# Kernel optimization log

Measured on AMD Instinct MI355X. Metric: run time of the kernel, lower is better.

## Reference

```python
import jax, jax.numpy as jnp
import numpy as np

B, T = 256, 256
D_TEXT, D_AUDIO, D_VISION = 300, 74, 35
D = D_TEXT + D_AUDIO + D_VISION  # 409
H = 1024
CELL = 512
OUT = 1


def setup_inputs() -> dict:
    key = jax.random.key(0)
    ks = jax.random.split(key, 8)
    s_ih = 1.0 / np.sqrt(H)
    return {
        "x_text": jax.random.normal(ks[0], (B, T, D_TEXT), jnp.float32),
        "x_audio": jax.random.normal(ks[1], (B, T, D_AUDIO), jnp.float32),
        "x_vision": jax.random.normal(ks[2], (B, T, D_VISION), jnp.float32),
        "W_ih": jax.random.normal(ks[3], (4 * H, D), jnp.float32) * s_ih,
        "W_hh": jax.random.normal(ks[4], (4 * H, H), jnp.float32) * s_ih,
        "b_ih": jnp.zeros((4 * H,), jnp.float32),
        "b_hh": jnp.zeros((4 * H,), jnp.float32),
        "W1": jax.random.normal(ks[5], (CELL, H), jnp.float32) / np.sqrt(H),
        "b1": jnp.zeros((CELL,), jnp.float32),
        "W2": jax.random.normal(ks[6], (OUT, CELL), jnp.float32) / np.sqrt(CELL),
        "b2": jnp.zeros((OUT,), jnp.float32),
    }


def _lstm_mlp(x_text, x_audio, x_vision, W_ih, W_hh, b_ih, b_hh, W1, b1, W2, b2):
    # concat modalities along feature dim: [B, T, D]
    x = jnp.concatenate([x_text, x_audio, x_vision], axis=2)
    b = x.shape[0]
    h0 = jnp.zeros((b, H), x.dtype)
    c0 = jnp.zeros((b, H), x.dtype)
    # precompute input-to-gate projection for all timesteps: [T, B, 4H]
    xg = jnp.einsum('btd,gd->tbg', x, W_ih) + (b_ih + b_hh)

    def step(carry, xg_t):
        h, c = carry
        gates = xg_t + h @ W_hh.T  # [B, 4H]
        i, f, g, o = jnp.split(gates, 4, axis=-1)  # PyTorch LSTMCell gate order
        i = jax.nn.sigmoid(i)
        f = jax.nn.sigmoid(f)
        g = jnp.tanh(g)
        o = jax.nn.sigmoid(o)
        c = f * c + i * g
        h = o * jnp.tanh(c)
        return (h, c), None

    (h_last, _), _ = jax.lax.scan(step, (h0, c0), xg)
    # SimpleNet: Linear -> ReLU -> Dropout(eval: identity) -> Linear
    hidden = jax.nn.relu(h_last @ W1.T + b1)
    return hidden @ W2.T + b2  # [B, OUT]


def reference(x_text, x_audio, x_vision, W_ih, W_hh, b_ih, b_hh, W1, b1, W2, b2):
    return _lstm_mlp(x_text, x_audio, x_vision, W_ih, W_hh, b_ih, b_hh, W1, b1, W2, b2)
```

## Files before the change

### kernel.cpp

```cpp
#include <hip/hip_runtime.h>
#include <cstdint>
#include <cstddef>


typedef __attribute__((ext_vector_type(8))) short short8;
typedef __attribute__((ext_vector_type(4))) float f32x4;

#define MFMA_BF16(A,B,C) __builtin_amdgcn_mfma_f32_16x16x32_bf16((A),(B),(C),0,0,0)

#define OFF_FLAGS 0u
#define OFF_HBUF0 4096u
#define OFF_CBUF  528384u
#define ZERO_SPAN 1576960u
#define OFF_HBUF1 1576960u
#define OFF_HFIN  2101248u
#define OFF_HID   3149824u
#define OFF_BIAS  3674112u
#define OFF_WHH   3690496u
#define OFF_WIH   12079104u
#define OFF_XB    15486976u
#define OFF_XG    70012928u
#define WS_NEED   137121792ull

static __device__ __forceinline__ uint16_t f2bf(float f) {
  uint32_t u = __builtin_bit_cast(uint32_t, f);
  uint32_t r = u + 0x7FFFu + ((u >> 16) & 1u);
  return (uint16_t)(r >> 16);
}
static __device__ __forceinline__ float bf2f_lo(uint32_t u) {
  return __builtin_bit_cast(float, u << 16);
}
static __device__ __forceinline__ float bf2f_hi(uint32_t u) {
  return __builtin_bit_cast(float, u & 0xFFFF0000u);
}
static __device__ __forceinline__ float sigm(float x) {
  return 1.0f / (1.0f + __expf(-x));
}
static __device__ __forceinline__ float tanh_f(float x) {
  float e = __expf(2.0f * x);
  return 1.0f - 2.0f / (e + 1.0f);
}
static __device__ __forceinline__ void gld_lds16_coh(const void* gsrc, void* ldst) {
  __builtin_amdgcn_global_load_lds(
      (const __attribute__((address_space(1))) uint32_t*)gsrc,
      (__attribute__((address_space(3))) uint32_t*)ldst, 16, 0, 0x11);
}

__global__ __launch_bounds__(256) void pack_xb_kernel(
    const float* __restrict__ xt, const float* __restrict__ xa,
    const float* __restrict__ xv, uint16_t* __restrict__ xb)
{
  int id = blockIdx.x * 256 + threadIdx.x;
  int lane = id & 63;
  int rem  = id >> 6;
  int ks = rem % 13;
  int mt = rem / 13;
  int m = mt * 16 + (lane & 15);
  int t = m >> 8;
  int b = m & 255;
  int k0 = ks * 32 + (lane >> 4) * 8;
  size_t base = (size_t)b * 256 + t;
  uint16_t vals[8];
#pragma unroll
  for (int e = 0; e < 8; ++e) {
    int k = k0 + e;
    float v;
    if (k < 300)      v = xt[base * 300 + k];
    else if (k < 374) v = xa[base * 74  + (k - 300)];
    else if (k < 409) v = xv[base * 35  + (k - 374)];
    else              v = 0.0f;
    vals[e] = f2bf(v);
  }
  uint32_t* d32 = (uint32_t*)(xb + (size_t)id * 8);
#pragma unroll
  for (int i = 0; i < 4; ++i)
    d32[i] = (uint32_t)vals[2*i] | ((uint32_t)vals[2*i+1] << 16);
}

__global__ __launch_bounds__(256) void pack_whh_kernel(
    const float* __restrict__ whh, uint16_t* __restrict__ wp)
{
  int id = blockIdx.x * 256 + threadIdx.x;
  int lane = id & 63;
  int ks = (id >> 6) & 31;
  int q  = (id >> 11) & 3;
  int s  = id >> 13;
  int row = q * 1024 + s * 16 + (lane & 15);
  int k0 = ks * 32 + (lane >> 4) * 8;
  const float* src = whh + (size_t)row * 1024 + k0;
  uint16_t vals[8];
#pragma unroll
  for (int e = 0; e < 8; ++e) vals[e] = f2bf(src[e]);
  uint32_t* d32 = (uint32_t*)(wp + (size_t)id * 8);
#pragma unroll
  for (int i = 0; i < 4; ++i)
    d32[i] = (uint32_t)vals[2*i] | ((uint32_t)vals[2*i+1] << 16);
}

__global__ __launch_bounds__(256) void pack_wih_kernel(
    const float* __restrict__ wih, uint16_t* __restrict__ wp)
{
  int id = blockIdx.x * 256 + threadIdx.x;
  int lane = id & 63;
  int rem = id >> 6;
  int ks = rem % 13;
  int nt = rem / 13;
  int n = nt * 16 + (lane & 15);
  int k0 = ks * 32 + (lane >> 4) * 8;
  uint16_t vals[8];
#pragma unroll
  for (int e = 0; e < 8; ++e) {
    int k = k0 + e;
    vals[e] = (k < 409) ? f2bf(wih[(size_t)n * 409 + k]) : (uint16_t)0;
  }
  uint32_t* d32 = (uint32_t*)(wp + (size_t)id * 8);
#pragma unroll
  for (int i = 0; i < 4; ++i)
    d32[i] = (uint32_t)vals[2*i] | ((uint32_t)vals[2*i+1] << 16);
}

__global__ __launch_bounds__(256) void pack_bias_kernel(
    const float* __restrict__ b_ih, const float* __restrict__ b_hh,
    float* __restrict__ bias)
{
  int id = blockIdx.x * 256 + threadIdx.x;
  bias[id] = b_ih[id] + b_hh[id];
}

__global__ __launch_bounds__(256) void xg_gemm_kernel(
    const short8* __restrict__ xb, const short8* __restrict__ wih,
    const float* __restrict__ bias, uint2* __restrict__ xg, int chunk)
{
  int tid = threadIdx.x;
  int lane = tid & 63;
  int w = tid >> 6;
  int wm = w & 1, wn = w >> 1;
  int bm = blockIdx.x, bn = blockIdx.y;
  int mtb = bm * 8 + wm * 4;
  int ntb = bn * 8 + wn * 4;
  int col = lane & 15;

  f32x4 acc[4][4];
#pragma unroll
  for (int b = 0; b < 4; ++b) {
    float bv = bias[(ntb + b) * 16 + col];
    f32x4 v = {bv, bv, bv, bv};
#pragma unroll
    for (int a = 0; a < 4; ++a) acc[a][b] = v;
  }
  size_t mt_glob = (size_t)chunk * 512 + mtb;
  for (int ks = 0; ks < 13; ++ks) {
    short8 Af[4], Bf[4];
#pragma unroll
    for (int a = 0; a < 4; ++a)
      Af[a] = xb[((mt_glob + a) * 13 + ks) * 64 + lane];
#pragma unroll
    for (int b = 0; b < 4; ++b)
      Bf[b] = wih[(((size_t)(ntb + b)) * 13 + ks) * 64 + lane];
#pragma unroll
    for (int a = 0; a < 4; ++a)
#pragma unroll
      for (int b = 0; b < 4; ++b)
        acc[a][b] = MFMA_BF16(Af[a], Bf[b], acc[a][b]);
  }
#pragma unroll
  for (int a = 0; a < 4; ++a) {
    int mt = mtb + a;
    int t_loc = mt >> 4;
    int bt = mt & 15;
#pragma unroll
    for (int b = 0; b < 4; ++b) {
      size_t idx = (((size_t)t_loc * 256 + (ntb + b)) * 16 + bt) * 64 + lane;
      f32x4 v = acc[a][b];
      uint2 o;
      o.x = (uint32_t)f2bf(v[0]) | ((uint32_t)f2bf(v[1]) << 16);
      o.y = (uint32_t)f2bf(v[2]) | ((uint32_t)f2bf(v[3]) << 16);
      xg[idx] = o;
    }
  }
}

__global__ __launch_bounds__(256, 1) void scan_kernel(
    const uint16_t* __restrict__ whh_p, const uint2* __restrict__ xg,
    uint16_t* __restrict__ hbuf0, uint16_t* __restrict__ hbuf1,
    float* __restrict__ c_buf, float* __restrict__ h_final,
    uint32_t* flags, int chunk)
{
  extern __shared__ char smem[];
  float* gl = (float*)(smem + 131072);

  const int tid = threadIdx.x;
  const int bid = blockIdx.x;
  const int g = bid >> 6, s = bid & 63;
  const int lane = tid & 63, w = tid >> 6;

  const short8* wstream = (const short8*)(whh_p + (size_t)s * 65536)
                          + ((size_t)w * 32) * 64 + lane;

  const int row_e = tid >> 2;
  const int j_e = (tid & 3) * 4;
  const int R_e = g * 64 + row_e;
  const int col_e = s * 16 + j_e;
  f32x4 c4 = *(const f32x4*)(c_buf + (size_t)R_e * 1024 + col_e);

  size_t hstore_base;
  {
    int cg0 = col_e;
    int ksh = cg0 >> 5, quad = (cg0 >> 3) & 3, e0 = cg0 & 7;
    int mth = row_e >> 4;
    int laneh = quad * 16 + (row_e & 15);
    hstore_base = (((size_t)(g * 4 + mth) * 32 + ksh) * 64 + laneh) * 8 + e0;
  }

  const short8* Afrag = (const short8*)smem;
  const int myflag = g * 64 + lane;

  uint2 xp[4];
#pragma unroll
  for (int a = 0; a < 4; ++a)
    xp[a] = xg[(((size_t)0 * 256 + (w * 64 + s)) * 16 + (g * 4 + a)) * 64 + lane];

  for (int l = 0; l < 32; ++l) {
    const int ts = chunk * 32 + l;
    const uint16_t* hin = (ts & 1) ? hbuf1 : hbuf0;
    uint16_t* hout = (ts & 1) ? hbuf0 : hbuf1;

    {
      const uint16_t* gbase = hin + (size_t)g * 65536
                              + (size_t)(w * 32) * 512 + (size_t)lane * 8;
      char* lbase = smem + (size_t)(w * 32) * 1024;
#pragma unroll
      for (int p = 0; p < 32; ++p)
        gld_lds16_coh(gbase + (size_t)p * 512, lbase + p * 1024);
    }

    f32x4 acc[4];
#pragma unroll
    for (int a = 0; a < 4; ++a) {
      uint2 p = xp[a];
      f32x4 v = {bf2f_lo(p.x), bf2f_hi(p.x), bf2f_lo(p.y), bf2f_hi(p.y)};
      acc[a] = v;
    }

    __syncthreads();

#pragma unroll
    for (int ks = 0; ks < 32; ++ks) {
      short8 W = wstream[ks * 64];
      short8 A0 = Afrag[(0 * 32 + ks) * 64 + lane];
      short8 A1 = Afrag[(1 * 32 + ks) * 64 + lane];
      short8 A2 = Afrag[(2 * 32 + ks) * 64 + lane];
      short8 A3 = Afrag[(3 * 32 + ks) * 64 + lane];
      acc[0] = MFMA_BF16(A0, W, acc[0]);
      acc[1] = MFMA_BF16(A1, W, acc[1]);
      acc[2] = MFMA_BF16(A2, W, acc[2]);
      acc[3] = MFMA_BF16(A3, W, acc[3]);
    }

    {
      int r0 = (lane >> 4) * 4;
      int cc = lane & 15;
      int colc = w * 16 + cc;
#pragma unroll
      for (int a = 0; a < 4; ++a)
#pragma unroll
        for (int r = 0; r < 4; ++r)
          gl[(a * 16 + r0 + r) * 68 + colc] = acc[a][r];
    }
    __syncthreads();

    float hv[4];
#pragma unroll
    for (int u = 0; u < 4; ++u) {
      int cj = j_e + u;
      float xi = gl[row_e * 68 + cj];
      float xf = gl[row_e * 68 + 16 + cj];
      float xg_ = gl[row_e * 68 + 32 + cj];
      float xo = gl[row_e * 68 + 48 + cj];
      float cn = sigm(xf) * c4[u] + sigm(xi) * tanh_f(xg_);
      c4[u] = cn;
      hv[u] = sigm(xo) * tanh_f(cn);
    }
    {
      uint32_t w0 = (uint32_t)f2bf(hv[0]) | ((uint32_t)f2bf(hv[1]) << 16);
      uint32_t w1 = (uint32_t)f2bf(hv[2]) | ((uint32_t)f2bf(hv[3]) << 16);
      unsigned long long v = ((unsigned long long)w1 << 32) | w0;
      __hip_atomic_store((unsigned long long*)(hout + hstore_base), v,
                         __ATOMIC_RELAXED, __HIP_MEMORY_SCOPE_AGENT);
    }
    if (chunk == 7 && l == 31) {
      f32x4 hh = {hv[0], hv[1], hv[2], hv[3]};
      *(f32x4*)(h_final + (size_t)R_e * 1024 + col_e) = hh;
    }
    if (l != 31) {
      __syncthreads();
      if (tid == 0) {
        __hip_atomic_store(&flags[bid], (uint32_t)(ts + 1),
                           __ATOMIC_RELAXED, __HIP_MEMORY_SCOPE_AGENT);
      }
      {
        int ln = l + 1;
#pragma unroll
        for (int a = 0; a < 4; ++a)
          xp[a] = xg[(((size_t)ln * 256 + (w * 64 + s)) * 16 + (g * 4 + a)) * 64 + lane];
      }
      while (__hip_atomic_load(&flags[myflag], __ATOMIC_RELAXED,
                               __HIP_MEMORY_SCOPE_AGENT) < (uint32_t)(ts + 1)) {
        __builtin_amdgcn_s_sleep(1);
      }
    }
  }
  *(f32x4*)(c_buf + (size_t)R_e * 1024 + col_e) = c4;
}

__global__ __launch_bounds__(256) void mlp1_kernel(
    const float* __restrict__ h_final, const float* __restrict__ W1,
    const float* __restrict__ b1, float* __restrict__ hidden)
{
  __shared__ float hl[8 * 1024];
  __shared__ float part[4 * 64 * 8];
  int tid = threadIdx.x;
  int rb = blockIdx.x;
  int cb = blockIdx.y;
  const f32x4* hsrc = (const f32x4*)(h_final + (size_t)rb * 8 * 1024);
  for (int i = tid; i < 2048; i += 256) ((f32x4*)hl)[i] = hsrc[i];
  __syncthreads();
  int cell_l = tid & 63;
  int kq = tid >> 6;
  int cell = cb * 64 + cell_l;
  float accv[8] = {0,0,0,0,0,0,0,0};
  const f32x4* wrow = (const f32x4*)(W1 + (size_t)cell * 1024) + kq * 64;
  const f32x4* hl4 = (const f32x4*)hl;
  for (int k4 = 0; k4 < 64; ++k4) {
    f32x4 wv = wrow[k4];
    int kidx = kq * 64 + k4;
#pragma unroll
    for (int r = 0; r < 8; ++r) {
      f32x4 hv = hl4[r * 256 + kidx];
      accv[r] += wv[0] * hv[0] + wv[1] * hv[1] + wv[2] * hv[2] + wv[3] * hv[3];
    }
  }
#pragma unroll
  for (int r = 0; r < 8; ++r) part[(kq * 64 + cell_l) * 8 + r] = accv[r];
  __syncthreads();
#pragma unroll
  for (int rr = 0; rr < 2; ++rr) {
    int r = kq * 2 + rr;
    float sum = b1[cell];
    for (int q = 0; q < 4; ++q) sum += part[(q * 64 + cell_l) * 8 + r];
    hidden[(size_t)(rb * 8 + r) * 512 + cell] = fmaxf(sum, 0.0f);
  }
}

__global__ __launch_bounds__(256) void mlp2_kernel(
    const float* __restrict__ hidden, const float* __restrict__ W2,
    const float* __restrict__ b2, float* __restrict__ out)
{
  __shared__ float w2l[512];
  int tid = threadIdx.x;
  for (int i = tid; i < 512; i += 256) w2l[i] = W2[i];
  __syncthreads();
  const f32x4* hrow = (const f32x4*)(hidden + (size_t)tid * 512);
  const f32x4* w4 = (const f32x4*)w2l;
  float acc = b2[0];
  for (int k = 0; k < 128; ++k) {
    f32x4 a = hrow[k], b = w4[k];
    acc += a[0] * b[0] + a[1] * b[1] + a[2] * b[2] + a[3] * b[3];
  }
  out[tid] = acc;
}

extern "C" void kernel_launch(void* const* d_in, const int* in_sizes, int n_in,
                              void* d_out, int out_size, void* d_ws, size_t ws_size,
                              hipStream_t stream)
{
  (void)in_sizes; (void)n_in; (void)out_size;
  if (ws_size < WS_NEED) return;

  const float* xt   = (const float*)d_in[0];
  const float* xa   = (const float*)d_in[1];
  const float* xv   = (const float*)d_in[2];
  const float* W_ih = (const float*)d_in[3];
  const float* W_hh = (const float*)d_in[4];
  const float* b_ih = (const float*)d_in[5];
  const float* b_hh = (const float*)d_in[6];
  const float* W1   = (const float*)d_in[7];
  const float* b1   = (const float*)d_in[8];
  const float* W2   = (const float*)d_in[9];
  const float* b2   = (const float*)d_in[10];
  float* out = (float*)d_out;
  char* ws = (char*)d_ws;

  uint32_t* flags   = (uint32_t*)(ws + OFF_FLAGS);
  uint16_t* hb0     = (uint16_t*)(ws + OFF_HBUF0);
  uint16_t* hb1     = (uint16_t*)(ws + OFF_HBUF1);
  float*    c_buf   = (float*)(ws + OFF_CBUF);
  float*    h_final = (float*)(ws + OFF_HFIN);
  float*    hidden  = (float*)(ws + OFF_HID);
  float*    bias    = (float*)(ws + OFF_BIAS);
  uint16_t* whh_p   = (uint16_t*)(ws + OFF_WHH);
  uint16_t* wih_p   = (uint16_t*)(ws + OFF_WIH);
  uint16_t* xb      = (uint16_t*)(ws + OFF_XB);
  uint2*    xg      = (uint2*)(ws + OFF_XG);

  hipFuncSetAttribute((const void*)scan_kernel,
                      hipFuncAttributeMaxDynamicSharedMemorySize, 148480);

  hipMemsetAsync(ws, 0, ZERO_SPAN, stream);

  pack_xb_kernel  <<<13312, 256, 0, stream>>>(xt, xa, xv, xb);
  pack_whh_kernel <<<2048,  256, 0, stream>>>(W_hh, whh_p);
  pack_wih_kernel <<<832,   256, 0, stream>>>(W_ih, wih_p);
  pack_bias_kernel<<<16,    256, 0, stream>>>(b_ih, b_hh, bias);

  for (int c = 0; c < 8; ++c) {
    xg_gemm_kernel<<<dim3(64, 32), 256, 0, stream>>>(
        (const short8*)xb, (const short8*)wih_p, bias, xg, c);
    scan_kernel<<<256, 256, 148480, stream>>>(
        whh_p, xg, hb0, hb1, c_buf, h_final, flags, c);
  }
  mlp1_kernel<<<dim3(32, 8), 256, 0, stream>>>(h_final, W1, b1, hidden);
  mlp2_kernel<<<1, 256, 0, stream>>>(hidden, W2, b2, out);
}
```

Before: 2.038 ms.

## Fuse input projection GEMM into persistent LSTM scan kernel

Removes the separate xg_gemm kernel and its chunked launch loop. The scan kernel now keeps W_ih fragments in registers and computes each timestep's input projection with MFMAs while it waits on the cross-block flag. Everything runs in one persistent launch over 256 timesteps. This drops the xg workspace round trip, seven kernel relaunches and the c_buf save and restore, at the cost of extra registers and extra MFMA work between recurrent steps.

```diff
diff --git a/kernel.cpp b/kernel.cpp
--- a/kernel.cpp
+++ b/kernel.cpp
@@ -10,28 +10,20 @@
 
 #define OFF_FLAGS 0u
 #define OFF_HBUF0 4096u
-#define OFF_CBUF  528384u
-#define ZERO_SPAN 1576960u
-#define OFF_HBUF1 1576960u
-#define OFF_HFIN  2101248u
-#define OFF_HID   3149824u
-#define OFF_BIAS  3674112u
-#define OFF_WHH   3690496u
-#define OFF_WIH   12079104u
-#define OFF_XB    15486976u
-#define OFF_XG    70012928u
-#define WS_NEED   137121792ull
+#define ZERO_SPAN 528384u
+#define OFF_HBUF1 528384u
+#define OFF_HFIN  1052672u
+#define OFF_HID   2101248u
+#define OFF_BIAS  2625536u
+#define OFF_WHH   2641920u
+#define OFF_WIH   11030528u
+#define OFF_XB    14438400u
+#define WS_NEED   68964352ull
 
 static __device__ __forceinline__ uint16_t f2bf(float f) {
   uint32_t u = __builtin_bit_cast(uint32_t, f);
   uint32_t r = u + 0x7FFFu + ((u >> 16) & 1u);
   return (uint16_t)(r >> 16);
-}
-static __device__ __forceinline__ float bf2f_lo(uint32_t u) {
-  return __builtin_bit_cast(float, u << 16);
-}
-static __device__ __forceinline__ float bf2f_hi(uint32_t u) {
-  return __builtin_bit_cast(float, u & 0xFFFF0000u);
 }
 static __device__ __forceinline__ float sigm(float x) {
   return 1.0f / (1.0f + __expf(-x));
@@ -127,64 +119,11 @@
   bias[id] = b_ih[id] + b_hh[id];
 }
 
-__global__ __launch_bounds__(256) void xg_gemm_kernel(
-    const short8* __restrict__ xb, const short8* __restrict__ wih,
-    const float* __restrict__ bias, uint2* __restrict__ xg, int chunk)
-{
-  int tid = threadIdx.x;
-  int lane = tid & 63;
-  int w = tid >> 6;
-  int wm = w & 1, wn = w >> 1;
-  int bm = blockIdx.x, bn = blockIdx.y;
-  int mtb = bm * 8 + wm * 4;
-  int ntb = bn * 8 + wn * 4;
-  int col = lane & 15;
-
-  f32x4 acc[4][4];
-#pragma unroll
-  for (int b = 0; b < 4; ++b) {
-    float bv = bias[(ntb + b) * 16 + col];
-    f32x4 v = {bv, bv, bv, bv};
-#pragma unroll
-    for (int a = 0; a < 4; ++a) acc[a][b] = v;
-  }
-  size_t mt_glob = (size_t)chunk * 512 + mtb;
-  for (int ks = 0; ks < 13; ++ks) {
-    short8 Af[4], Bf[4];
-#pragma unroll
-    for (int a = 0; a < 4; ++a)
-      Af[a] = xb[((mt_glob + a) * 13 + ks) * 64 + lane];
-#pragma unroll
-    for (int b = 0; b < 4; ++b)
-      Bf[b] = wih[(((size_t)(ntb + b)) * 13 + ks) * 64 + lane];
-#pragma unroll
-    for (int a = 0; a < 4; ++a)
-#pragma unroll
-      for (int b = 0; b < 4; ++b)
-        acc[a][b] = MFMA_BF16(Af[a], Bf[b], acc[a][b]);
-  }
-#pragma unroll
-  for (int a = 0; a < 4; ++a) {
-    int mt = mtb + a;
-    int t_loc = mt >> 4;
-    int bt = mt & 15;
-#pragma unroll
-    for (int b = 0; b < 4; ++b) {
-      size_t idx = (((size_t)t_loc * 256 + (ntb + b)) * 16 + bt) * 64 + lane;
-      f32x4 v = acc[a][b];
-      uint2 o;
-      o.x = (uint32_t)f2bf(v[0]) | ((uint32_t)f2bf(v[1]) << 16);
-      o.y = (uint32_t)f2bf(v[2]) | ((uint32_t)f2bf(v[3]) << 16);
-      xg[idx] = o;
-    }
-  }
-}
-
 __global__ __launch_bounds__(256, 1) void scan_kernel(
-    const uint16_t* __restrict__ whh_p, const uint2* __restrict__ xg,
+    const uint16_t* __restrict__ whh_p, const short8* __restrict__ xb,
+    const short8* __restrict__ wih, const float* __restrict__ bias,
     uint16_t* __restrict__ hbuf0, uint16_t* __restrict__ hbuf1,
-    float* __restrict__ c_buf, float* __restrict__ h_final,
-    uint32_t* flags, int chunk)
+    float* __restrict__ h_final, uint32_t* flags)
 {
   extern __shared__ char smem[];
   float* gl = (float*)(smem + 131072);
@@ -201,7 +140,7 @@
   const int j_e = (tid & 3) * 4;
   const int R_e = g * 64 + row_e;
   const int col_e = s * 16 + j_e;
-  f32x4 c4 = *(const f32x4*)(c_buf + (size_t)R_e * 1024 + col_e);
+  f32x4 c4 = {0.0f, 0.0f, 0.0f, 0.0f};
 
   size_t hstore_base;
   {
@@ -215,13 +154,29 @@
   const short8* Afrag = (const short8*)smem;
   const int myflag = g * 64 + lane;
 
-  uint2 xp[4];
-#pragma unroll
-  for (int a = 0; a < 4; ++a)
-    xp[a] = xg[(((size_t)0 * 256 + (w * 64 + s)) * 16 + (g * 4 + a)) * 64 + lane];
-
-  for (int l = 0; l < 32; ++l) {
-    const int ts = chunk * 32 + l;
+  const int nt = w * 64 + s;
+  short8 Bih[13];
+  {
+    const short8* bsrc = wih + ((size_t)nt * 13) * 64 + lane;
+#pragma unroll
+    for (int ks = 0; ks < 13; ++ks) Bih[ks] = bsrc[ks * 64];
+  }
+  const float bv = bias[nt * 16 + (lane & 15)];
+
+  f32x4 xacc[4];
+  {
+    const short8* abase = xb + (((size_t)g * 4) * 13) * 64 + lane;
+#pragma unroll
+    for (int a = 0; a < 4; ++a) { f32x4 v = {bv, bv, bv, bv}; xacc[a] = v; }
+#pragma unroll
+    for (int ks = 0; ks < 13; ++ks)
+#pragma unroll
+      for (int a = 0; a < 4; ++a)
+        xacc[a] = MFMA_BF16(abase[((size_t)a * 13 + ks) * 64], Bih[ks], xacc[a]);
+  }
+
+#pragma unroll 1
+  for (int ts = 0; ts < 256; ++ts) {
     const uint16_t* hin = (ts & 1) ? hbuf1 : hbuf0;
     uint16_t* hout = (ts & 1) ? hbuf0 : hbuf1;
 
@@ -236,11 +191,7 @@
 
     f32x4 acc[4];
 #pragma unroll
-    for (int a = 0; a < 4; ++a) {
-      uint2 p = xp[a];
-      f32x4 v = {bf2f_lo(p.x), bf2f_hi(p.x), bf2f_lo(p.y), bf2f_hi(p.y)};
-      acc[a] = v;
-    }
+    for (int a = 0; a < 4; ++a) acc[a] = xacc[a];
 
     __syncthreads();
 
@@ -288,21 +239,26 @@
       __hip_atomic_store((unsigned long long*)(hout + hstore_base), v,
                          __ATOMIC_RELAXED, __HIP_MEMORY_SCOPE_AGENT);
     }
-    if (chunk == 7 && l == 31) {
+    if (ts == 255) {
       f32x4 hh = {hv[0], hv[1], hv[2], hv[3]};
       *(f32x4*)(h_final + (size_t)R_e * 1024 + col_e) = hh;
-    }
-    if (l != 31) {
+    } else {
       __syncthreads();
       if (tid == 0) {
         __hip_atomic_store(&flags[bid], (uint32_t)(ts + 1),
                            __ATOMIC_RELAXED, __HIP_MEMORY_SCOPE_AGENT);
       }
       {
-        int ln = l + 1;
-#pragma unroll
-        for (int a = 0; a < 4; ++a)
-          xp[a] = xg[(((size_t)ln * 256 + (w * 64 + s)) * 16 + (g * 4 + a)) * 64 + lane];
+        const short8* abase =
+            xb + (((size_t)(ts + 1) * 16 + g * 4) * 13) * 64 + lane;
+#pragma unroll
+        for (int a = 0; a < 4; ++a) { f32x4 v = {bv, bv, bv, bv}; xacc[a] = v; }
+#pragma unroll
+        for (int ks = 0; ks < 13; ++ks)
+#pragma unroll
+          for (int a = 0; a < 4; ++a)
+            xacc[a] =
+                MFMA_BF16(abase[((size_t)a * 13 + ks) * 64], Bih[ks], xacc[a]);
       }
       while (__hip_atomic_load(&flags[myflag], __ATOMIC_RELAXED,
                                __HIP_MEMORY_SCOPE_AGENT) < (uint32_t)(ts + 1)) {
@@ -310,7 +266,6 @@
       }
     }
   }
-  *(f32x4*)(c_buf + (size_t)R_e * 1024 + col_e) = c4;
 }
 
 __global__ __launch_bounds__(256) void mlp1_kernel(
@@ -394,14 +349,12 @@
   uint32_t* flags   = (uint32_t*)(ws + OFF_FLAGS);
   uint16_t* hb0     = (uint16_t*)(ws + OFF_HBUF0);
   uint16_t* hb1     = (uint16_t*)(ws + OFF_HBUF1);
-  float*    c_buf   = (float*)(ws + OFF_CBUF);
   float*    h_final = (float*)(ws + OFF_HFIN);
   float*    hidden  = (float*)(ws + OFF_HID);
   float*    bias    = (float*)(ws + OFF_BIAS);
   uint16_t* whh_p   = (uint16_t*)(ws + OFF_WHH);
   uint16_t* wih_p   = (uint16_t*)(ws + OFF_WIH);
   uint16_t* xb      = (uint16_t*)(ws + OFF_XB);
-  uint2*    xg      = (uint2*)(ws + OFF_XG);
 
   hipFuncSetAttribute((const void*)scan_kernel,
                       hipFuncAttributeMaxDynamicSharedMemorySize, 148480);
@@ -413,12 +366,10 @@
   pack_wih_kernel <<<832,   256, 0, stream>>>(W_ih, wih_p);
   pack_bias_kernel<<<16,    256, 0, stream>>>(b_ih, b_hh, bias);
 
-  for (int c = 0; c < 8; ++c) {
-    xg_gemm_kernel<<<dim3(64, 32), 256, 0, stream>>>(
-        (const short8*)xb, (const short8*)wih_p, bias, xg, c);
-    scan_kernel<<<256, 256, 148480, stream>>>(
-        whh_p, xg, hb0, hb1, c_buf, h_final, flags, c);
-  }
+  scan_kernel<<<256, 256, 148480, stream>>>(
+      whh_p, (const short8*)xb, (const short8*)wih_p, bias,
+      hb0, hb1, h_final, flags);
+
   mlp1_kernel<<<dim3(32, 8), 256, 0, stream>>>(h_final, W1, b1, hidden);
   mlp2_kernel<<<1, 256, 0, stream>>>(hidden, W2, b2, out);
 }
```

Measured after the change: 4.294 ms. +110.7%, slower.
